# Kernel optimization log

Hardware: AMD Instinct MI355X
Metric: run time of the kernel (lower is better)

## Reference

```python
import jax, jax.numpy as jnp
import numpy as np
from jax import lax


def _maxpool_nchw(x, k):
    # Non-overlapping kxk max pool over the last two dims (NCHW).
    return lax.reduce_window(x, -jnp.inf, lax.max,
                             window_dimensions=(1, 1, k, k),
                             window_strides=(1, 1, k, k),
                             padding='VALID')


def setup_inputs() -> dict:
    key = jax.random.key(0)
    k1, k2, k3, k4, k5 = jax.random.split(key, 5)
    B = 16
    return {
        'input_tensor1': jax.random.normal(k1, (B, 128, 48, 48), jnp.float32),
        'input_tensor2': jax.random.normal(k2, (B, 64, 96, 96), jnp.float32),
        'input_tensor3': jax.random.normal(k3, (B, 32, 192, 192), jnp.float32),
        'input_tensor4': jax.random.normal(k4, (B, 16, 384, 384), jnp.float32),
        'pure_ff': jax.random.normal(k5, (B, 256, 24, 24), jnp.float32),
    }


def reference(input_tensor1, input_tensor2, input_tensor3, input_tensor4, pure_ff):
    # and then max-pools. Pooling is per-channel, so this equals pooling once
    # and tiling the pooled result along the channel axis -- same math,
    # without materializing the redundant concat intermediates.
    x1 = jnp.tile(_maxpool_nchw(input_tensor1, 2), (1, 2, 1, 1))   # [B,256,24,24]
    x2 = jnp.tile(_maxpool_nchw(input_tensor2, 4), (1, 4, 1, 1))   # [B,256,24,24]
    x3 = jnp.tile(_maxpool_nchw(input_tensor3, 8), (1, 8, 1, 1))   # [B,256,24,24]
    x4 = jnp.tile(_maxpool_nchw(input_tensor4, 16), (1, 16, 1, 1)) # [B,256,24,24]
    return jax.nn.relu(x1 + x2 + x3 + x4 + pure_ff)
```

## Files before the change

### kernel.cpp

```cpp
#include <hip/hip_runtime.h>
#include <math.h>


namespace {

constexpr int OHW = 24;

__device__ __forceinline__ float fmax4(const float4 v) {
  return fmaxf(fmaxf(v.x, v.y), fmaxf(v.z, v.w));
}

__global__ __launch_bounds__(256, 3) void fused_block(const float* __restrict__ x1,
                                                      const float* __restrict__ x2,
                                                      const float* __restrict__ x3,
                                                      const float* __restrict__ x4,
                                                      const float* __restrict__ ff,
                                                      float* __restrict__ out) {
  __shared__ __attribute__((aligned(16))) float s1[128 * 12];
  __shared__ __attribute__((aligned(16))) float s2[64 * 12];
  __shared__ __attribute__((aligned(16))) float s3[32 * 12];
  __shared__ __attribute__((aligned(16))) float s4[16 * 12];

  const int blk  = blockIdx.x;
  const int b    = blk / 48;
  const int rem  = blk % 48;
  const int oh   = rem >> 1;
  const int half = rem & 1;
  const int tid  = threadIdx.x;

  {
    const float* base = x1 + (size_t)b * 128 * 2304 + oh * 2 * 48 + half * 24;
#pragma unroll
    for (int it = 0; it < 3; ++it) {
      const int t  = it * 256 + tid;
      const int ch = t / 6, pid = t % 6;
      const float* p = base + (size_t)ch * 2304 + pid * 4;
      const float4 a = *reinterpret_cast<const float4*>(p);
      const float4 c = *reinterpret_cast<const float4*>(p + 48);
      s1[ch * 12 + pid * 2]     = fmaxf(fmaxf(a.x, a.y), fmaxf(c.x, c.y));
      s1[ch * 12 + pid * 2 + 1] = fmaxf(fmaxf(a.z, a.w), fmaxf(c.z, c.w));
    }
  }

  {
    const float* base = x2 + (size_t)b * 64 * 9216 + oh * 4 * 96 + half * 48;
#pragma unroll
    for (int it = 0; it < 3; ++it) {
      const int t  = it * 256 + tid;
      const int ch = t / 12, ow = t % 12;
      const float* p = base + (size_t)ch * 9216 + ow * 4;
      float m = -INFINITY;
#pragma unroll
      for (int r = 0; r < 4; ++r)
        m = fmaxf(m, fmax4(*reinterpret_cast<const float4*>(p + r * 96)));
      s2[ch * 12 + ow] = m;
    }
  }

  {
    const float* base = x3 + (size_t)b * 32 * 36864 + oh * 8 * 192 + half * 96;
#pragma unroll
    for (int it = 0; it < 3; ++it) {
      const int t  = it * 256 + tid;
      const int ch = t / 24, ow = (t % 24) >> 1, hf = t & 1;
      const float* p = base + (size_t)ch * 36864 + ow * 8 + hf * 4;
      float m = -INFINITY;
#pragma unroll
      for (int r = 0; r < 8; ++r)
        m = fmaxf(m, fmax4(*reinterpret_cast<const float4*>(p + r * 192)));
      m = fmaxf(m, __shfl_xor(m, 1));
      if (hf == 0) s3[ch * 12 + ow] = m;
    }
  }

  {
    const float* base = x4 + (size_t)b * 16 * 147456 + oh * 16 * 384 + half * 192;
#pragma unroll
    for (int it = 0; it < 3; ++it) {
      const int t  = it * 256 + tid;
      const int ch = t / 48, ow = (t % 48) >> 2, q = t & 3;
      const float* p = base + (size_t)ch * 147456 + ow * 16 + q * 4;
      float m = -INFINITY;
#pragma unroll
      for (int r = 0; r < 16; ++r)
        m = fmaxf(m, fmax4(*reinterpret_cast<const float4*>(p + r * 384)));
      m = fmaxf(m, __shfl_xor(m, 1));
      m = fmaxf(m, __shfl_xor(m, 2));
      if (q == 0) s4[ch * 12 + ow] = m;
    }
  }

  __syncthreads();

  {
    const size_t obase = (size_t)b * 256 * 576 + oh * OHW + half * 12;
#pragma unroll
    for (int it = 0; it < 3; ++it) {
      const int t = it * 256 + tid;
      const int c = t / 3, q = (t % 3) * 4;
      const float4 a1 = *reinterpret_cast<const float4*>(&s1[(c & 127) * 12 + q]);
      const float4 a2 = *reinterpret_cast<const float4*>(&s2[(c & 63)  * 12 + q]);
      const float4 a3 = *reinterpret_cast<const float4*>(&s3[(c & 31)  * 12 + q]);
      const float4 a4 = *reinterpret_cast<const float4*>(&s4[(c & 15)  * 12 + q]);
      const size_t o  = obase + (size_t)c * 576 + q;
      const float4 f  = *reinterpret_cast<const float4*>(ff + o);
      float4 r;
      r.x = fmaxf((((a1.x + a2.x) + a3.x) + a4.x) + f.x, 0.0f);
      r.y = fmaxf((((a1.y + a2.y) + a3.y) + a4.y) + f.y, 0.0f);
      r.z = fmaxf((((a1.z + a2.z) + a3.z) + a4.z) + f.z, 0.0f);
      r.w = fmaxf((((a1.w + a2.w) + a3.w) + a4.w) + f.w, 0.0f);
      *reinterpret_cast<float4*>(out + o) = r;
    }
  }
}

}

extern "C" void kernel_launch(void* const* d_in, const int* in_sizes, int n_in,
                              void* d_out, int out_size, void* d_ws, size_t ws_size,
                              hipStream_t stream) {
  const float* x1 = (const float*)d_in[0];
  const float* x2 = (const float*)d_in[1];
  const float* x3 = (const float*)d_in[2];
  const float* x4 = (const float*)d_in[3];
  const float* ff = (const float*)d_in[4];
  float* out = (float*)d_out;
  (void)d_ws; (void)ws_size; (void)in_sizes; (void)n_in; (void)out_size;

  fused_block<<<768, 256, 0, stream>>>(x1, x2, x3, x4, ff, out);
}
```

Before: 314.3 us.

## Split each output row into quarters and interleave all four pooling stages

Each block now covers a quarter of an output row, which doubles the grid to 1536 blocks. The four input pooling stages are merged into one loop where different threads handle different inputs, and all loads for a window are issued before the max reductions. The min-occupancy launch bound is dropped. The goal is more blocks and more memory requests in flight to better saturate HBM, at the cost of narrower 24-byte row segments per channel, float2 stores, and possible warp divergence at the stage boundaries.

```diff
diff --git a/kernel.cpp b/kernel.cpp
--- a/kernel.cpp
+++ b/kernel.cpp
@@ -4,113 +4,98 @@
 
 namespace {
 
-constexpr int OHW = 24;
-
 __device__ __forceinline__ float fmax4(const float4 v) {
   return fmaxf(fmaxf(v.x, v.y), fmaxf(v.z, v.w));
 }
+__device__ __forceinline__ float4 ld4(const float* p) {
+  return *reinterpret_cast<const float4*>(p);
+}
 
-__global__ __launch_bounds__(256, 3) void fused_block(const float* __restrict__ x1,
-                                                      const float* __restrict__ x2,
-                                                      const float* __restrict__ x3,
-                                                      const float* __restrict__ x4,
-                                                      const float* __restrict__ ff,
-                                                      float* __restrict__ out) {
-  __shared__ __attribute__((aligned(16))) float s1[128 * 12];
-  __shared__ __attribute__((aligned(16))) float s2[64 * 12];
-  __shared__ __attribute__((aligned(16))) float s3[32 * 12];
-  __shared__ __attribute__((aligned(16))) float s4[16 * 12];
+__global__ __launch_bounds__(256) void fused_block(const float* __restrict__ x1,
+                                                   const float* __restrict__ x2,
+                                                   const float* __restrict__ x3,
+                                                   const float* __restrict__ x4,
+                                                   const float* __restrict__ ff,
+                                                   float* __restrict__ out) {
+  __shared__ __attribute__((aligned(16))) float s1[128 * 6];
+  __shared__ __attribute__((aligned(16))) float s2[64 * 6];
+  __shared__ __attribute__((aligned(16))) float s3[32 * 6];
+  __shared__ __attribute__((aligned(16))) float s4[16 * 6];
 
-  const int blk  = blockIdx.x;
-  const int b    = blk / 48;
-  const int rem  = blk % 48;
-  const int oh   = rem >> 1;
-  const int half = rem & 1;
-  const int tid  = threadIdx.x;
+  const int blk = blockIdx.x;
+  const int b   = blk / 96;
+  const int rem = blk % 96;
+  const int oh  = rem >> 2;
+  const int q4  = rem & 3;
+  const int tid = threadIdx.x;
 
-  {
-    const float* base = x1 + (size_t)b * 128 * 2304 + oh * 2 * 48 + half * 24;
 #pragma unroll
-    for (int it = 0; it < 3; ++it) {
-      const int t  = it * 256 + tid;
-      const int ch = t / 6, pid = t % 6;
-      const float* p = base + (size_t)ch * 2304 + pid * 4;
-      const float4 a = *reinterpret_cast<const float4*>(p);
-      const float4 c = *reinterpret_cast<const float4*>(p + 48);
-      s1[ch * 12 + pid * 2]     = fmaxf(fmaxf(a.x, a.y), fmaxf(c.x, c.y));
-      s1[ch * 12 + pid * 2 + 1] = fmaxf(fmaxf(a.z, a.w), fmaxf(c.z, c.w));
-    }
-  }
-
-  {
-    const float* base = x2 + (size_t)b * 64 * 9216 + oh * 4 * 96 + half * 48;
+  for (int it = 0; it < 6; ++it) {
+    const int t = it * 256 + tid;
+    if (t < 384) {
+      const int ch = t / 3, pid = t % 3;
+      const float* p = x1 + (size_t)(b * 128 + ch) * 2304 + oh * 2 * 48 + q4 * 12 + pid * 4;
+      float4 v[2];
+      v[0] = ld4(p);
+      v[1] = ld4(p + 48);
+      s1[ch * 6 + pid * 2]     = fmaxf(fmaxf(v[0].x, v[0].y), fmaxf(v[1].x, v[1].y));
+      s1[ch * 6 + pid * 2 + 1] = fmaxf(fmaxf(v[0].z, v[0].w), fmaxf(v[1].z, v[1].w));
+    } else if (t < 768) {
+      const int u = t - 384;
+      const int ch = u / 6, ow = u % 6;
+      const float* p = x2 + (size_t)(b * 64 + ch) * 9216 + oh * 4 * 96 + (q4 * 6 + ow) * 4;
+      float4 v[4];
 #pragma unroll
-    for (int it = 0; it < 3; ++it) {
-      const int t  = it * 256 + tid;
-      const int ch = t / 12, ow = t % 12;
-      const float* p = base + (size_t)ch * 9216 + ow * 4;
+      for (int r = 0; r < 4; ++r) v[r] = ld4(p + r * 96);
+      float m = fmaxf(fmaxf(fmax4(v[0]), fmax4(v[1])), fmaxf(fmax4(v[2]), fmax4(v[3])));
+      s2[ch * 6 + ow] = m;
+    } else if (t < 1152) {
+      const int u = t - 768;
+      const int ch = u / 12, r2 = u % 12, ow = r2 >> 1, hf = r2 & 1;
+      const float* p = x3 + (size_t)(b * 32 + ch) * 36864 + oh * 8 * 192 + (q4 * 6 + ow) * 8 + hf * 4;
+      float4 v[8];
+#pragma unroll
+      for (int r = 0; r < 8; ++r) v[r] = ld4(p + r * 192);
       float m = -INFINITY;
 #pragma unroll
-      for (int r = 0; r < 4; ++r)
-        m = fmaxf(m, fmax4(*reinterpret_cast<const float4*>(p + r * 96)));
-      s2[ch * 12 + ow] = m;
-    }
-  }
-
-  {
-    const float* base = x3 + (size_t)b * 32 * 36864 + oh * 8 * 192 + half * 96;
-#pragma unroll
-    for (int it = 0; it < 3; ++it) {
-      const int t  = it * 256 + tid;
-      const int ch = t / 24, ow = (t % 24) >> 1, hf = t & 1;
-      const float* p = base + (size_t)ch * 36864 + ow * 8 + hf * 4;
+      for (int r = 0; r < 8; ++r) m = fmaxf(m, fmax4(v[r]));
+      m = fmaxf(m, __shfl_xor(m, 1));
+      if (hf == 0) s3[ch * 6 + ow] = m;
+    } else {
+      const int u = t - 1152;
+      const int ch = u / 24, r2 = u % 24, ow = r2 >> 2, qq = r2 & 3;
+      const float* p = x4 + (size_t)(b * 16 + ch) * 147456 + oh * 16 * 384 + (q4 * 6 + ow) * 16 + qq * 4;
       float m = -INFINITY;
 #pragma unroll
-      for (int r = 0; r < 8; ++r)
-        m = fmaxf(m, fmax4(*reinterpret_cast<const float4*>(p + r * 192)));
-      m = fmaxf(m, __shfl_xor(m, 1));
-      if (hf == 0) s3[ch * 12 + ow] = m;
-    }
-  }
-
-  {
-    const float* base = x4 + (size_t)b * 16 * 147456 + oh * 16 * 384 + half * 192;
+      for (int g = 0; g < 2; ++g) {
+        float4 v[8];
 #pragma unroll
-    for (int it = 0; it < 3; ++it) {
-      const int t  = it * 256 + tid;
-      const int ch = t / 48, ow = (t % 48) >> 2, q = t & 3;
-      const float* p = base + (size_t)ch * 147456 + ow * 16 + q * 4;
-      float m = -INFINITY;
+        for (int r = 0; r < 8; ++r) v[r] = ld4(p + (g * 8 + r) * 384);
 #pragma unroll
-      for (int r = 0; r < 16; ++r)
-        m = fmaxf(m, fmax4(*reinterpret_cast<const float4*>(p + r * 384)));
+        for (int r = 0; r < 8; ++r) m = fmaxf(m, fmax4(v[r]));
+      }
       m = fmaxf(m, __shfl_xor(m, 1));
       m = fmaxf(m, __shfl_xor(m, 2));
-      if (q == 0) s4[ch * 12 + ow] = m;
+      if (qq == 0) s4[ch * 6 + ow] = m;
     }
   }
 
   __syncthreads();
 
-  {
-    const size_t obase = (size_t)b * 256 * 576 + oh * OHW + half * 12;
 #pragma unroll
-    for (int it = 0; it < 3; ++it) {
-      const int t = it * 256 + tid;
-      const int c = t / 3, q = (t % 3) * 4;
-      const float4 a1 = *reinterpret_cast<const float4*>(&s1[(c & 127) * 12 + q]);
-      const float4 a2 = *reinterpret_cast<const float4*>(&s2[(c & 63)  * 12 + q]);
-      const float4 a3 = *reinterpret_cast<const float4*>(&s3[(c & 31)  * 12 + q]);
-      const float4 a4 = *reinterpret_cast<const float4*>(&s4[(c & 15)  * 12 + q]);
-      const size_t o  = obase + (size_t)c * 576 + q;
-      const float4 f  = *reinterpret_cast<const float4*>(ff + o);
-      float4 r;
-      r.x = fmaxf((((a1.x + a2.x) + a3.x) + a4.x) + f.x, 0.0f);
-      r.y = fmaxf((((a1.y + a2.y) + a3.y) + a4.y) + f.y, 0.0f);
-      r.z = fmaxf((((a1.z + a2.z) + a3.z) + a4.z) + f.z, 0.0f);
-      r.w = fmaxf((((a1.w + a2.w) + a3.w) + a4.w) + f.w, 0.0f);
-      *reinterpret_cast<float4*>(out + o) = r;
-    }
+  for (int it = 0; it < 3; ++it) {
+    const int e = it * 256 + tid;
+    const int c = e / 3, cp = e % 3;
+    const float2 a1 = *reinterpret_cast<const float2*>(&s1[(c & 127) * 6 + cp * 2]);
+    const float2 a2 = *reinterpret_cast<const float2*>(&s2[(c & 63)  * 6 + cp * 2]);
+    const float2 a3 = *reinterpret_cast<const float2*>(&s3[(c & 31)  * 6 + cp * 2]);
+    const float2 a4 = *reinterpret_cast<const float2*>(&s4[(c & 15)  * 6 + cp * 2]);
+    const size_t o = (size_t)(b * 256 + c) * 576 + oh * 24 + q4 * 6 + cp * 2;
+    const float2 f = *reinterpret_cast<const float2*>(ff + o);
+    float2 r;
+    r.x = fmaxf((((a1.x + a2.x) + a3.x) + a4.x) + f.x, 0.0f);
+    r.y = fmaxf((((a1.y + a2.y) + a3.y) + a4.y) + f.y, 0.0f);
+    *reinterpret_cast<float2*>(out + o) = r;
   }
 }
 
@@ -127,5 +112,5 @@
   float* out = (float*)d_out;
   (void)d_ws; (void)ws_size; (void)in_sizes; (void)n_in; (void)out_size;
 
-  fused_block<<<768, 256, 0, stream>>>(x1, x2, x3, x4, ff, out);
+  fused_block<<<1536, 256, 0, stream>>>(x1, x2, x3, x4, ff, out);
 }
```

New measurement: 324.3 us. 1.03x slower.
